# Optimization experiments

Measured on AMD Instinct MI355X. Metric: run time of the kernel, lower is better.

The kernel has to match this reference:

```python
import jax, jax.numpy as jnp
import numpy as np

N = 100000

def _gcn_norm(edge_index, n):
    row, col = edge_index[0], edge_index[1]
    deg = jnp.zeros((n,), jnp.float32).at[col].add(1.0)
    dinv = jnp.where(deg > 0, jax.lax.rsqrt(jnp.maximum(deg, 1.0)), 0.0)
    return dinv[row] * dinv[col]


def _arma_conv(x, row, col, norm, init_w, w, root_w, bias):
    # x: [N, Fin]; init_w: [K, Fin, F]; w: [T-1, K, F, F]; root_w: [T, K, Fin, F]; bias: [T, K, 1, F]
    out = jnp.einsum('nf,kfg->kng', x, init_w)  # [K, N, F]
    T = root_w.shape[0]
    for t in range(T):
        if t > 0:
            out = jnp.einsum('kng,kgh->knh', out, w[t - 1])
        msg = out[:, row, :] * norm[None, :, None]          # [K, E, F] gather
        out = jnp.zeros_like(out).at[:, col, :].add(msg)    # scatter-add to targets
        out = out + jnp.einsum('nf,kfg->kng', x, root_w[t]) + bias[t]
        out = jax.nn.relu(out)
    return out.mean(axis=0)  # average over stacks K


def setup_inputs() -> dict:
    key = jax.random.key(0)
    ks = jax.random.split(key, 12)
    E, Fin, H, C, K = 1600000, 128, 64, 41, 2
    s = 0.1
    return {
        'x': jax.random.normal(ks[0], (N, Fin), jnp.float32),
        'edge_index': jax.random.randint(ks[1], (2, E), 0, N, jnp.int64),
        'w1_init': jax.random.normal(ks[2], (K, Fin, H), jnp.float32) * s,
        'w1': jax.random.normal(ks[3], (1, K, H, H), jnp.float32) * s,
        'w1_root': jax.random.normal(ks[4], (2, K, Fin, H), jnp.float32) * s,
        'b1': jax.random.normal(ks[5], (2, K, 1, H), jnp.float32) * s,
        'w2_init': jax.random.normal(ks[6], (K, H, C), jnp.float32) * s,
        'w2': jax.random.normal(ks[7], (1, K, C, C), jnp.float32) * s,
        'w2_root': jax.random.normal(ks[8], (2, K, H, C), jnp.float32) * s,
        'b2': jax.random.normal(ks[9], (2, K, 1, C), jnp.float32) * s,
    }


def reference(x, edge_index, w1_init, w1, w1_root, b1, w2_init, w2, w2_root, b2):
    row, col = edge_index[0], edge_index[1]
    norm = _gcn_norm(edge_index, N)
    h = jax.nn.relu(_arma_conv(x, row, col, norm, w1_init, w1, w1_root, b1))
    # F.dropout is identity in eval mode
    h = _arma_conv(h, row, col, norm, w2_init, w2, w2_root, b2)
    return jax.nn.log_softmax(h, axis=1)
```

## Files before the change

kernel.cpp:

```cpp
#include <hip/hip_runtime.h>
#include <math.h>

#define TPB 256
typedef unsigned short ushort_t;
typedef unsigned int uint_t;
typedef __attribute__((ext_vector_type(8))) short bf16x8;
typedef __attribute__((ext_vector_type(4))) float f32x4;

__device__ __forceinline__ float bf2f(ushort_t h) {
    return __uint_as_float(((uint_t)h) << 16);
}
__device__ __forceinline__ ushort_t f2bf(float f) {
    uint_t u = __float_as_uint(f);
    u += 0x7fff + ((u >> 16) & 1);
    return (ushort_t)(u >> 16);
}
__device__ __forceinline__ uint_t pack2(float x, float y) {
    return (uint_t)f2bf(x) | ((uint_t)f2bf(y) << 16);
}

#define SWZ_A 32768
#define SWZ_B 24576
#define SWZ_C 12288
#define SWZ_D 12288

__global__ __launch_bounds__(256)
void pre1(const int* __restrict__ col, int* __restrict__ cnt, unsigned short* __restrict__ pos,
          int E, int nEb,
          const float* __restrict__ w1_init, const float* __restrict__ w1,
          const float* __restrict__ w1_root, const float* __restrict__ w2_init,
          const float* __restrict__ w2, const float* __restrict__ w2_root,
          short* __restrict__ swzdst, int nSb,
          const float4* __restrict__ x, uint2* __restrict__ xh, int n4) {
    int b = blockIdx.x;
    if (b < nEb) {
        int e = b * 256 + threadIdx.x;
        if (e < E) pos[e] = (unsigned short)atomicAdd(&cnt[col[e]], 1);
        return;
    }
    if (b < nEb + nSb) {
        int idx = (b - nEb) * 256 + threadIdx.x;
        int region, base, CH, CT;
        if (idx < SWZ_A)                          { region = 0; base = 0; CH = 4; CT = 8; }
        else if (idx < SWZ_A + SWZ_B)             { region = 1; base = SWZ_A; CH = 6; CT = 4; }
        else if (idx < SWZ_A + SWZ_B + SWZ_C)     { region = 2; base = SWZ_A + SWZ_B; CH = 2; CT = 6; }
        else if (idx < SWZ_A + SWZ_B + SWZ_C + SWZ_D)
                                                  { region = 3; base = SWZ_A + SWZ_B + SWZ_C; CH = 4; CT = 3; }
        else return;
        int r = idx - base;
        int j = r & 7, ln = (r >> 3) & 63;
        int rest = r >> 9;
        int ct = rest % CT, c = (rest / CT) % CH, k = rest / (CT * CH);
        int colm = ct * 16 + (ln & 15);
        int kl = (ln >> 4) * 8 + j;
        float v = 0.0f;
        if (region == 0) {
            int kk = c * 32 + kl;
            if (colm < 64)       v = w1_init[((size_t)k * 128 + kk) * 64 + colm];
            else                 v = w1_root[((size_t)k * 128 + kk) * 64 + (colm - 64)];
        } else if (region == 1) {
            if (c < 2) { int kk = c * 32 + kl;        v = w1[((size_t)k * 64 + kk) * 64 + colm]; }
            else       { int kk = (c - 2) * 32 + kl;  v = w1_root[((size_t)(2 + k) * 128 + kk) * 64 + colm]; }
        } else if (region == 2) {
            int kk = c * 32 + kl;
            if (colm < 48) { if (colm < 41)           v = w2_init[((size_t)k * 64 + kk) * 41 + colm]; }
            else           { int c2 = colm - 48; if (c2 < 41) v = w2_root[((size_t)k * 64 + kk) * 41 + c2]; }
        } else {
            if (c < 2) { int kk = c * 32 + kl;       if (kk < 41 && colm < 41) v = w2[((size_t)k * 41 + kk) * 41 + colm]; }
            else       { int kk = (c - 2) * 32 + kl; if (colm < 41)            v = w2_root[((size_t)(2 + k) * 64 + kk) * 41 + colm]; }
        }
        swzdst[(size_t)base + r] = (short)f2bf(v);
        return;
    }
    int i = (b - nEb - nSb) * 256 + threadIdx.x;
    if (i < n4) {
        float4 v = x[i];
        xh[i] = make_uint2(pack2(v.x, v.y), pack2(v.z, v.w));
    }
}

__global__ void scan_block(const int* __restrict__ cnt, int* __restrict__ incl,
                           int* __restrict__ bsum, int N) {
    __shared__ int s[TPB];
    int i = blockIdx.x * TPB + threadIdx.x;
    s[threadIdx.x] = (i < N) ? ((cnt[i] + 3) & ~3) : 0;
    __syncthreads();
    for (int d = 1; d < TPB; d <<= 1) {
        int t = (threadIdx.x >= d) ? s[threadIdx.x - d] : 0;
        __syncthreads();
        s[threadIdx.x] += t;
        __syncthreads();
    }
    if (i < N) incl[i] = s[threadIdx.x];
    if (threadIdx.x == TPB - 1) bsum[blockIdx.x] = s[TPB - 1];
}

__global__ void scan_bsums(int* __restrict__ bsum, int nb) {
    __shared__ int s[512];
    int t = threadIdx.x;
    int v = (t < nb) ? bsum[t] : 0;
    s[t] = v;
    __syncthreads();
    for (int d = 1; d < 512; d <<= 1) {
        int u = (t >= d) ? s[t - d] : 0;
        __syncthreads();
        s[t] += u;
        __syncthreads();
    }
    if (t < nb) bsum[t] = s[t] - v;
}

__global__ void finalize_csr(const int* __restrict__ incl, const int* __restrict__ bsum,
                             const int* __restrict__ cnt, int* __restrict__ rowstart,
                             float* __restrict__ dinv, int N) {
    int i = blockIdx.x * TPB + threadIdx.x;
    if (i < N) {
        rowstart[i + 1] = incl[i] + bsum[blockIdx.x];
        int d = cnt[i];
        dinv[i] = (d > 0) ? rsqrtf((float)d) : 0.0f;
    }
    if (i == 0) rowstart[0] = 0;
}

__global__ void fill_csr(const int* __restrict__ row, const int* __restrict__ col,
                         const int* __restrict__ rowstart, const unsigned short* __restrict__ pos,
                         int* __restrict__ srcidx, int E) {
    int e = blockIdx.x * blockDim.x + threadIdx.x;
    if (e < E) srcidx[rowstart[col[e]] + (int)pos[e]] = row[e];
}

__global__ void pad_csr(const int* __restrict__ rowstart, const int* __restrict__ cnt,
                        int* __restrict__ srcidx, int N) {
    int i = blockIdx.x * blockDim.x + threadIdx.x;
    if (i >= N) return;
    int b = rowstart[i] + cnt[i], en = rowstart[i + 1];
    for (int e = b; e < en; ++e) srcidx[e] = N;
}

template<int CT, int CTA, int CH>
__global__ __launch_bounds__(256, 4)
void gemm_t0(const ushort_t* __restrict__ s2, int s2s, const short* __restrict__ fragbuf,
             const float* __restrict__ biasB, const float* __restrict__ dinv,
             int FB, int N, uint_t* __restrict__ pre, uint_t* __restrict__ outH) {
    constexpr int PP = (CT - CTA) * 8;
    constexpr int PA = CTA * 8;
    const int k = blockIdx.y;
    const int n0 = blockIdx.x * 128;
    const int t = threadIdx.x;
    const int w = t >> 6, lane = t & 63, quad = lane >> 4, lr = lane & 15;
    const short* fb = fragbuf + (size_t)k * CH * CT * 512;

    int r0 = n0 + w * 32 + lr;
    int m0 = r0 < N ? r0 : N - 1;
    int m1 = (r0 + 16) < N ? (r0 + 16) : N - 1;

    bf16x8 a0v[CH], a1v[CH];
#pragma unroll
    for (int c = 0; c < CH; ++c) {
        int off = c * 32 + quad * 8;
        a0v[c] = *(const bf16x8*)&s2[(size_t)m0 * s2s + off];
        a1v[c] = *(const bf16x8*)&s2[(size_t)m1 * s2s + off];
    }

    __shared__ short lds_b[CH * CT * 512];
    {
        constexpr int CHUNKS = CH * CT * 64;
#pragma unroll
        for (int i = 0; i < (CHUNKS + 255) / 256; ++i) {
            int idx = i * 256 + t;
            if (CHUNKS % 256 == 0 || idx < CHUNKS)
                *(bf16x8*)&lds_b[idx * 8] = *(const bf16x8*)&fb[(size_t)idx * 8];
        }
    }
    __syncthreads();

    f32x4 acc[2][CT];
#pragma unroll
    for (int rt = 0; rt < 2; ++rt)
#pragma unroll
        for (int ct = 0; ct < CT; ++ct) acc[rt][ct] = (f32x4){0.f, 0.f, 0.f, 0.f};

#pragma unroll
    for (int c = 0; c < CH; ++c) {
#pragma unroll
        for (int ct = 0; ct < CT; ++ct) {
            bf16x8 bfr = *(const bf16x8*)&lds_b[((size_t)c * CT + ct) * 512 + lane * 8];
            acc[0][ct] = __builtin_amdgcn_mfma_f32_16x16x32_bf16(a0v[c], bfr, acc[0][ct], 0, 0, 0);
            acc[1][ct] = __builtin_amdgcn_mfma_f32_16x16x32_bf16(a1v[c], bfr, acc[1][ct], 0, 0, 0);
        }
    }

#pragma unroll
    for (int rt = 0; rt < 2; ++rt) {
#pragma unroll
        for (int i = 0; i < 4; ++i) {
            int n = n0 + w * 32 + rt * 16 + quad * 4 + i;
            if (n >= N) continue;
            float dnv = dinv[n];
#pragma unroll
            for (int ct = 0; ct < CT; ++ct) {
                int col = ct * 16 + lr;
                float v = acc[rt][ct][i];
                if (ct < CTA) {
                    v *= dnv;
                } else {
                    int c2 = col - CTA * 16;
                    if (c2 < FB) v += biasB[(size_t)k * FB + c2];
                }
                float vn = __shfl_xor(v, 1);
                uint_t p = pack2(v, vn);
                uint_t p2 = __shfl_xor(p, 2);
                if (!(lr & 3)) {
                    if (ct < CTA) {
                        *(uint2*)&outH[((size_t)n * 2 + k) * PA + (col >> 1)] = make_uint2(p, p2);
                    } else {
                        int c2 = col - CTA * 16;
                        *(uint2*)&pre[((size_t)n * 2 + k) * PP + (c2 >> 1)] = make_uint2(p, p2);
                    }
                }
            }
        }
    }
}

__global__ __launch_bounds__(256, 3)
void gemm_t1_l1(const ushort_t* __restrict__ s1, const ushort_t* __restrict__ xh,
                const short* __restrict__ fragbuf, const float* __restrict__ bias,
                int N, uint_t* __restrict__ hhU) {
    constexpr int CT = 4, CH = 6;
    const int n0 = blockIdx.x * 128;
    const int t = threadIdx.x;
    const int w = t >> 6, lane = t & 63, quad = lane >> 4, lr = lane & 15;

    int r0 = n0 + w * 32 + lr;
    int m0 = r0 < N ? r0 : N - 1;
    int m1 = (r0 + 16) < N ? (r0 + 16) : N - 1;

    bf16x8 s0a[2][2], s1a[2][2];
    bf16x8 x0a[4], x1a[4];
#pragma unroll
    for (int c = 0; c < 2; ++c) {
        int off = c * 32 + quad * 8;
#pragma unroll
        for (int kk = 0; kk < 2; ++kk) {
            s0a[c][kk] = *(const bf16x8*)&s1[((size_t)m0 * 2 + kk) * 64 + off];
            s1a[c][kk] = *(const bf16x8*)&s1[((size_t)m1 * 2 + kk) * 64 + off];
        }
    }
#pragma unroll
    for (int c = 0; c < 4; ++c) {
        int off = c * 32 + quad * 8;
        x0a[c] = *(const bf16x8*)&xh[(size_t)m0 * 128 + off];
        x1a[c] = *(const bf16x8*)&xh[(size_t)m1 * 128 + off];
    }

    __shared__ short lds_b[2 * CH * CT * 512];
    {
        constexpr int CHUNKS = 2 * CH * CT * 64;
#pragma unroll
        for (int i = 0; i < CHUNKS / 256; ++i) {
            int idx = i * 256 + t;
            *(bf16x8*)&lds_b[idx * 8] = *(const bf16x8*)&fragbuf[(size_t)idx * 8];
        }
    }
    __syncthreads();

    f32x4 acc[2][2][CT];
#pragma unroll
    for (int k = 0; k < 2; ++k)
#pragma unroll
        for (int rt = 0; rt < 2; ++rt)
#pragma unroll
            for (int ct = 0; ct < CT; ++ct) acc[k][rt][ct] = (f32x4){0.f, 0.f, 0.f, 0.f};

#pragma unroll
    for (int c = 0; c < CH; ++c) {
#pragma unroll
        for (int k = 0; k < 2; ++k) {
            bf16x8 a0 = (c < 2) ? s0a[c][k] : x0a[c - 2];
            bf16x8 a1 = (c < 2) ? s1a[c][k] : x1a[c - 2];
#pragma unroll
            for (int ct = 0; ct < CT; ++ct) {
                bf16x8 b = *(const bf16x8*)&lds_b[(((size_t)k * CH + c) * CT + ct) * 512 + lane * 8];
                acc[k][0][ct] = __builtin_amdgcn_mfma_f32_16x16x32_bf16(a0, b, acc[k][0][ct], 0, 0, 0);
                acc[k][1][ct] = __builtin_amdgcn_mfma_f32_16x16x32_bf16(a1, b, acc[k][1][ct], 0, 0, 0);
            }
        }
    }

#pragma unroll
    for (int rt = 0; rt < 2; ++rt) {
#pragma unroll
        for (int i = 0; i < 4; ++i) {
            int n = n0 + w * 32 + rt * 16 + quad * 4 + i;
            if (n >= N) continue;
#pragma unroll
            for (int ct = 0; ct < CT; ++ct) {
                int col = ct * 16 + lr;
                float v0 = fmaxf(acc[0][rt][ct][i] + bias[col], 0.0f);
                float v1 = fmaxf(acc[1][rt][ct][i] + bias[64 + col], 0.0f);
                float m = 0.5f * (v0 + v1);
                float mn = __shfl_xor(m, 1);
                uint_t p = pack2(m, mn);
                uint_t p2 = __shfl_xor(p, 2);
                if (!(lr & 3)) *(uint2*)&hhU[(size_t)n * 32 + (col >> 1)] = make_uint2(p, p2);
            }
        }
    }
}

__global__ __launch_bounds__(256, 3)
void gemm_t1_l2(const ushort_t* __restrict__ s1, const ushort_t* __restrict__ hh,
                const short* __restrict__ fragbuf, const float* __restrict__ bias,
                int N, float* __restrict__ out) {
    constexpr int CT = 3, CH = 4;
    const int n0 = blockIdx.x * 128;
    const int t = threadIdx.x;
    const int w = t >> 6, lane = t & 63, quad = lane >> 4, lr = lane & 15;

    int r0 = n0 + w * 32 + lr;
    int m0 = r0 < N ? r0 : N - 1;
    int m1 = (r0 + 16) < N ? (r0 + 16) : N - 1;

    bf16x8 s0a[2][2], s1a[2][2];
    bf16x8 h0a[2], h1a[2];
#pragma unroll
    for (int c = 0; c < 2; ++c) {
        int off = c * 32 + quad * 8;
#pragma unroll
        for (int kk = 0; kk < 2; ++kk) {
            s0a[c][kk] = *(const bf16x8*)&s1[((size_t)m0 * 2 + kk) * 48 + off];
            s1a[c][kk] = *(const bf16x8*)&s1[((size_t)m1 * 2 + kk) * 48 + off];
        }
    }
#pragma unroll
    for (int c = 0; c < 2; ++c) {
        int off = c * 32 + quad * 8;
        h0a[c] = *(const bf16x8*)&hh[(size_t)m0 * 64 + off];
        h1a[c] = *(const bf16x8*)&hh[(size_t)m1 * 64 + off];
    }

    __shared__ short lds_b[2 * CH * CT * 512];
    {
        constexpr int CHUNKS = 2 * CH * CT * 64;
#pragma unroll
        for (int i = 0; i < CHUNKS / 256; ++i) {
            int idx = i * 256 + t;
            *(bf16x8*)&lds_b[idx * 8] = *(const bf16x8*)&fragbuf[(size_t)idx * 8];
        }
    }
    __syncthreads();

    f32x4 acc[2][2][CT];
#pragma unroll
    for (int k = 0; k < 2; ++k)
#pragma unroll
        for (int rt = 0; rt < 2; ++rt)
#pragma unroll
            for (int ct = 0; ct < CT; ++ct) acc[k][rt][ct] = (f32x4){0.f, 0.f, 0.f, 0.f};

#pragma unroll
    for (int c = 0; c < CH; ++c) {
#pragma unroll
        for (int k = 0; k < 2; ++k) {
            bf16x8 a0 = (c < 2) ? s0a[c][k] : h0a[c - 2];
            bf16x8 a1 = (c < 2) ? s1a[c][k] : h1a[c - 2];
#pragma unroll
            for (int ct = 0; ct < CT; ++ct) {
                bf16x8 b = *(const bf16x8*)&lds_b[(((size_t)k * CH + c) * CT + ct) * 512 + lane * 8];
                acc[k][0][ct] = __builtin_amdgcn_mfma_f32_16x16x32_bf16(a0, b, acc[k][0][ct], 0, 0, 0);
                acc[k][1][ct] = __builtin_amdgcn_mfma_f32_16x16x32_bf16(a1, b, acc[k][1][ct], 0, 0, 0);
            }
        }
    }

#pragma unroll
    for (int rt = 0; rt < 2; ++rt) {
#pragma unroll
        for (int i = 0; i < 4; ++i) {
            int n = n0 + w * 32 + rt * 16 + quad * 4 + i;
            float m[CT];
            float mx = -1e30f;
#pragma unroll
            for (int ct = 0; ct < CT; ++ct) {
                int col = ct * 16 + lr;
                float b0 = (col < 41) ? bias[col] : 0.0f;
                float b1v = (col < 41) ? bias[41 + col] : 0.0f;
                float v0 = fmaxf(acc[0][rt][ct][i] + b0, 0.0f);
                float v1 = fmaxf(acc[1][rt][ct][i] + b1v, 0.0f);
                m[ct] = 0.5f * (v0 + v1);
                if (col < 41) mx = fmaxf(mx, m[ct]);
            }
#pragma unroll
            for (int msk = 1; msk < 16; msk <<= 1) mx = fmaxf(mx, __shfl_xor(mx, msk));
            float s = 0.0f;
#pragma unroll
            for (int ct = 0; ct < CT; ++ct) {
                int col = ct * 16 + lr;
                if (col < 41) s += __expf(m[ct] - mx);
            }
#pragma unroll
            for (int msk = 1; msk < 16; msk <<= 1) s += __shfl_xor(s, msk);
            float ls = __logf(s);
            if (n < N) {
#pragma unroll
                for (int ct = 0; ct < CT; ++ct) {
                    int col = ct * 16 + lr;
                    if (col < 41) out[(size_t)n * 41 + col] = m[ct] - mx - ls;
                }
            }
        }
    }
}

template<bool SCALE_OUT>
__global__ __launch_bounds__(256)
void gather32(const int* __restrict__ rowstart, const int* __restrict__ srcidx,
              const float* __restrict__ dinv, const uint_t* __restrict__ msg,
              const uint_t* __restrict__ pre, uint_t* __restrict__ outH, int N) {
    int gt = blockIdx.x * 256 + threadIdx.x;
    int n = gt >> 6;
    if (n >= N) return;
    const uint_t lo = (uint_t)(gt & 63);
    const int STR = 64;
    int beg = rowstart[n], end = rowstart[n + 1];
    float dn = dinv[n];
    size_t o = (size_t)n * STR + lo;
    uint_t p = 0;
    if (pre) p = pre[o];

    float ax0 = 0.f, ax1 = 0.f, ay0 = 0.f, ay1 = 0.f;
    int e = beg;
    for (; e + 8 <= end; e += 8) {
        int4 sa = *(const int4*)&srcidx[e];
        int4 sb = *(const int4*)&srcidx[e + 4];
        uint_t m0 = msg[(uint_t)(sa.x * STR) + lo];
        uint_t m1 = msg[(uint_t)(sa.y * STR) + lo];
        uint_t m2 = msg[(uint_t)(sa.z * STR) + lo];
        uint_t m3 = msg[(uint_t)(sa.w * STR) + lo];
        uint_t m4 = msg[(uint_t)(sb.x * STR) + lo];
        uint_t m5 = msg[(uint_t)(sb.y * STR) + lo];
        uint_t m6 = msg[(uint_t)(sb.z * STR) + lo];
        uint_t m7 = msg[(uint_t)(sb.w * STR) + lo];
        ax0 += __uint_as_float(m0 << 16); ay0 += __uint_as_float(m0 & 0xffff0000u);
        ax1 += __uint_as_float(m1 << 16); ay1 += __uint_as_float(m1 & 0xffff0000u);
        ax0 += __uint_as_float(m2 << 16); ay0 += __uint_as_float(m2 & 0xffff0000u);
        ax1 += __uint_as_float(m3 << 16); ay1 += __uint_as_float(m3 & 0xffff0000u);
        ax0 += __uint_as_float(m4 << 16); ay0 += __uint_as_float(m4 & 0xffff0000u);
        ax1 += __uint_as_float(m5 << 16); ay1 += __uint_as_float(m5 & 0xffff0000u);
        ax0 += __uint_as_float(m6 << 16); ay0 += __uint_as_float(m6 & 0xffff0000u);
        ax1 += __uint_as_float(m7 << 16); ay1 += __uint_as_float(m7 & 0xffff0000u);
    }
    if (e < end) {
        int4 sa = *(const int4*)&srcidx[e];
        uint_t m0 = msg[(uint_t)(sa.x * STR) + lo];
        uint_t m1 = msg[(uint_t)(sa.y * STR) + lo];
        uint_t m2 = msg[(uint_t)(sa.z * STR) + lo];
        uint_t m3 = msg[(uint_t)(sa.w * STR) + lo];
        ax0 += __uint_as_float(m0 << 16); ay0 += __uint_as_float(m0 & 0xffff0000u);
        ax1 += __uint_as_float(m1 << 16); ay1 += __uint_as_float(m1 & 0xffff0000u);
        ax0 += __uint_as_float(m2 << 16); ay0 += __uint_as_float(m2 & 0xffff0000u);
        ax1 += __uint_as_float(m3 << 16); ay1 += __uint_as_float(m3 & 0xffff0000u);
    }
    float ax = (ax0 + ax1) * dn;
    float ay = (ay0 + ay1) * dn;
    if (pre) {
        ax = fmaxf(ax + bf2f((ushort_t)p), 0.0f);
        ay = fmaxf(ay + bf2f((ushort_t)(p >> 16)), 0.0f);
    }
    if (SCALE_OUT) { ax *= dn; ay *= dn; }
    outH[o] = pack2(ax, ay);
}

template<bool SCALE_OUT>
__global__ __launch_bounds__(256)
void gather24(const int* __restrict__ rowstart, const int* __restrict__ srcidx,
              const float* __restrict__ dinv, const uint_t* __restrict__ msg,
              const uint_t* __restrict__ pre, uint_t* __restrict__ outH, int N) {
    int gt = blockIdx.x * 256 + threadIdx.x;
    int n = gt / 48;
    if (n >= N) return;
    const uint_t lo = (uint_t)(gt - n * 48);
    const int STR = 48;
    int beg = rowstart[n], end = rowstart[n + 1];
    float dn = dinv[n];
    size_t o = (size_t)n * STR + lo;
    uint_t p = 0;
    if (pre) p = pre[o];

    float ax0 = 0.f, ax1 = 0.f, ay0 = 0.f, ay1 = 0.f;
    int e = beg;
    for (; e + 8 <= end; e += 8) {
        int4 sa = *(const int4*)&srcidx[e];
        int4 sb = *(const int4*)&srcidx[e + 4];
        uint_t m0 = msg[(uint_t)(sa.x * STR) + lo];
        uint_t m1 = msg[(uint_t)(sa.y * STR) + lo];
        uint_t m2 = msg[(uint_t)(sa.z * STR) + lo];
        uint_t m3 = msg[(uint_t)(sa.w * STR) + lo];
        uint_t m4 = msg[(uint_t)(sb.x * STR) + lo];
        uint_t m5 = msg[(uint_t)(sb.y * STR) + lo];
        uint_t m6 = msg[(uint_t)(sb.z * STR) + lo];
        uint_t m7 = msg[(uint_t)(sb.w * STR) + lo];
        ax0 += __uint_as_float(m0 << 16); ay0 += __uint_as_float(m0 & 0xffff0000u);
        ax1 += __uint_as_float(m1 << 16); ay1 += __uint_as_float(m1 & 0xffff0000u);
        ax0 += __uint_as_float(m2 << 16); ay0 += __uint_as_float(m2 & 0xffff0000u);
        ax1 += __uint_as_float(m3 << 16); ay1 += __uint_as_float(m3 & 0xffff0000u);
        ax0 += __uint_as_float(m4 << 16); ay0 += __uint_as_float(m4 & 0xffff0000u);
        ax1 += __uint_as_float(m5 << 16); ay1 += __uint_as_float(m5 & 0xffff0000u);
        ax0 += __uint_as_float(m6 << 16); ay0 += __uint_as_float(m6 & 0xffff0000u);
        ax1 += __uint_as_float(m7 << 16); ay1 += __uint_as_float(m7 & 0xffff0000u);
    }
    if (e < end) {
        int4 sa = *(const int4*)&srcidx[e];
        uint_t m0 = msg[(uint_t)(sa.x * STR) + lo];
        uint_t m1 = msg[(uint_t)(sa.y * STR) + lo];
        uint_t m2 = msg[(uint_t)(sa.z * STR) + lo];
        uint_t m3 = msg[(uint_t)(sa.w * STR) + lo];
        ax0 += __uint_as_float(m0 << 16); ay0 += __uint_as_float(m0 & 0xffff0000u);
        ax1 += __uint_as_float(m1 << 16); ay1 += __uint_as_float(m1 & 0xffff0000u);
        ax0 += __uint_as_float(m2 << 16); ay0 += __uint_as_float(m2 & 0xffff0000u);
        ax1 += __uint_as_float(m3 << 16); ay1 += __uint_as_float(m3 & 0xffff0000u);
    }
    float ax = (ax0 + ax1) * dn;
    float ay = (ay0 + ay1) * dn;
    if (pre) {
        ax = fmaxf(ax + bf2f((ushort_t)p), 0.0f);
        ay = fmaxf(ay + bf2f((ushort_t)(p >> 16)), 0.0f);
    }
    if (SCALE_OUT) { ax *= dn; ay *= dn; }
    outH[o] = pack2(ax, ay);
}

extern "C" void kernel_launch(void* const* d_in, const int* in_sizes, int n_in,
                              void* d_out, int out_size, void* d_ws, size_t ws_size,
                              hipStream_t stream) {
    const float* x       = (const float*)d_in[0];
    const int*   ei      = (const int*)  d_in[1];
    const float* w1_init = (const float*)d_in[2];
    const float* w1      = (const float*)d_in[3];
    const float* w1_root = (const float*)d_in[4];
    const float* b1      = (const float*)d_in[5];
    const float* w2_init = (const float*)d_in[6];
    const float* w2      = (const float*)d_in[7];
    const float* w2_root = (const float*)d_in[8];
    const float* b2      = (const float*)d_in[9];

    const int Fin1 = 128;
    int N = in_sizes[0] / Fin1;
    int E = in_sizes[1] / 2;
    const int* row = ei;
    const int* col = ei + E;

    char* ws = (char*)d_ws;
    size_t off = 0;
    auto carve = [&](size_t bytes) -> void* {
        void* p = ws + off;
        off += (bytes + 255) & ~(size_t)255;
        return p;
    };
    int nblkN = (N + TPB - 1) / TPB;
    int*      cnt      = (int*)     carve((size_t)N * 4);
    int*      incl     = (int*)     carve((size_t)N * 4);
    int*      rowstart = (int*)     carve((size_t)(N + 1) * 4);
    int*      bsum     = (int*)     carve((size_t)nblkN * 4);
    float*    dinv     = (float*)   carve((size_t)N * 4);
    unsigned short* pos = (unsigned short*)carve((size_t)E * 2);
    int*      srcidx   = (int*)     carve((size_t)(E + 3 * (size_t)N + 64) * 4);
    short*    swz      = (short*)   carve((size_t)(SWZ_A + SWZ_B + SWZ_C + SWZ_D) * 2);
    ushort_t* xh       = (ushort_t*)carve((size_t)N * 128 * 2);
    ushort_t* hh       = (ushort_t*)carve((size_t)N * 64 * 2);
    ushort_t* b16A     = (ushort_t*)carve((size_t)N * 2 * 64 * 2 + 256);
    ushort_t* b16B     = (ushort_t*)carve((size_t)N * 2 * 64 * 2 + 256);
    uint_t*   pre      = (uint_t*)  carve((size_t)N * 2 * 32 * 4);

    hipMemsetAsync((char*)b16A + (size_t)N * 256, 0, 256, stream);
    hipMemsetAsync((char*)b16B + (size_t)N * 256, 0, 256, stream);
    hipMemsetAsync(cnt, 0, (size_t)N * 4, stream);

    int nEb = (E + TPB - 1) / TPB;
    int swztot = SWZ_A + SWZ_B + SWZ_C + SWZ_D;
    int nSb = (swztot + TPB - 1) / TPB;
    int n4 = N * 128 / 4;
    int nCb = (n4 + TPB - 1) / TPB;
    pre1<<<nEb + nSb + nCb, TPB, 0, stream>>>(col, cnt, pos, E, nEb,
                                              w1_init, w1, w1_root, w2_init, w2, w2_root,
                                              swz, nSb, (const float4*)x, (uint2*)xh, n4);

    scan_block  <<<nblkN, TPB, 0, stream>>>(cnt, incl, bsum, N);
    scan_bsums  <<<1, 512, 0, stream>>>(bsum, nblkN);
    finalize_csr<<<nblkN, TPB, 0, stream>>>(incl, bsum, cnt, rowstart, dinv, N);
    pad_csr     <<<nblkN, TPB, 0, stream>>>(rowstart, cnt, srcidx, N);
    fill_csr    <<<(E + TPB - 1) / TPB, TPB, 0, stream>>>(row, col, rowstart, pos, srcidx, E);

    const short* swzA = swz;
    const short* swzB = swz + SWZ_A;
    const short* swzC = swz + SWZ_A + SWZ_B;
    const short* swzD = swz + SWZ_A + SWZ_B + SWZ_C;
    dim3 gg2((N + 127) / 128, 2);
    dim3 gg1((N + 127) / 128, 1);
    int g32 = (N * 64 + TPB - 1) / TPB;
    int g24 = (N * 48 + TPB - 1) / TPB;

    gemm_t0<8, 4, 4><<<gg2, TPB, 0, stream>>>(xh, 128, swzA, b1, dinv, 64, N, pre, (uint_t*)b16A);
    gather32<true ><<<g32, TPB, 0, stream>>>(rowstart, srcidx, dinv, (const uint_t*)b16A,
                                             pre, (uint_t*)b16B, N);
    gather32<false><<<g32, TPB, 0, stream>>>(rowstart, srcidx, dinv, (const uint_t*)b16B,
                                             nullptr, (uint_t*)b16A, N);
    gemm_t1_l1<<<gg1, TPB, 0, stream>>>(b16A, xh, swzB, b1 + 2 * 64, N, (uint_t*)hh);

    hipMemsetAsync((char*)b16A + (size_t)N * 192, 0, 192, stream);
    hipMemsetAsync((char*)b16B + (size_t)N * 192, 0, 192, stream);

    gemm_t0<6, 3, 2><<<gg2, TPB, 0, stream>>>(hh, 64, swzC, b2, dinv, 41, N, pre, (uint_t*)b16A);
    gather24<true ><<<g24, TPB, 0, stream>>>(rowstart, srcidx, dinv, (const uint_t*)b16A,
                                             pre, (uint_t*)b16B, N);
    gather24<false><<<g24, TPB, 0, stream>>>(rowstart, srcidx, dinv, (const uint_t*)b16B,
                                             nullptr, (uint_t*)b16A, N);
    gemm_t1_l2<<<gg1, TPB, 0, stream>>>(b16A, hh, swzD, b2 + 2 * 41, N, (float*)d_out);
}
```

Baseline: 571.9 us.

## Fuse layer-1 final GEMM with layer-2 initial GEMM via LDS-staged activations

Merges the last layer-1 GEMM (producing hidden activations) with the first layer-2 GEMM in one kernel, keeping the block's hidden rows in shared memory instead of re-reading them from global memory. Buffer roles for the subsequent gathers are swapped accordingly. The gather kernel also broadcasts per-node CSR bounds and dinv via readfirstlane. This removes a launch and a global read at the cost of a longer kernel with higher register pressure and a relaxed occupancy hint.

```diff
diff --git a/kernel.cpp b/kernel.cpp
--- a/kernel.cpp
+++ b/kernel.cpp
@@ -223,14 +223,19 @@
     }
 }
 
-__global__ __launch_bounds__(256, 3)
-void gemm_t1_l1(const ushort_t* __restrict__ s1, const ushort_t* __restrict__ xh,
-                const short* __restrict__ fragbuf, const float* __restrict__ bias,
-                int N, uint_t* __restrict__ hhU) {
-    constexpr int CT = 4, CH = 6;
+__global__ __launch_bounds__(256)
+void gemm_mid(const ushort_t* __restrict__ s1, const ushort_t* __restrict__ xh,
+              const short* __restrict__ fragB1, const short* __restrict__ fragB2,
+              const float* __restrict__ bias1, const float* __restrict__ bias2,
+              const float* __restrict__ dinv, int N,
+              uint_t* __restrict__ hhU, uint_t* __restrict__ pre, uint_t* __restrict__ outH2) {
+    constexpr int CT1 = 4, CH1 = 6;
+    constexpr int CT2 = 6, CTA2 = 3, CH2 = 2;
     const int n0 = blockIdx.x * 128;
     const int t = threadIdx.x;
     const int w = t >> 6, lane = t & 63, quad = lane >> 4, lr = lane & 15;
+
+    __shared__ short lds[2 * CH1 * CT1 * 512];
 
     int r0 = n0 + w * 32 + lr;
     int m0 = r0 < N ? r0 : N - 1;
@@ -254,39 +259,42 @@
         x1a[c] = *(const bf16x8*)&xh[(size_t)m1 * 128 + off];
     }
 
-    __shared__ short lds_b[2 * CH * CT * 512];
     {
-        constexpr int CHUNKS = 2 * CH * CT * 64;
+        constexpr int CHUNKS = 2 * CH1 * CT1 * 64;
 #pragma unroll
         for (int i = 0; i < CHUNKS / 256; ++i) {
             int idx = i * 256 + t;
-            *(bf16x8*)&lds_b[idx * 8] = *(const bf16x8*)&fragbuf[(size_t)idx * 8];
+            *(bf16x8*)&lds[idx * 8] = *(const bf16x8*)&fragB1[(size_t)idx * 8];
         }
     }
     __syncthreads();
 
-    f32x4 acc[2][2][CT];
+    f32x4 acc[2][2][CT1];
 #pragma unroll
     for (int k = 0; k < 2; ++k)
 #pragma unroll
         for (int rt = 0; rt < 2; ++rt)
 #pragma unroll
-            for (int ct = 0; ct < CT; ++ct) acc[k][rt][ct] = (f32x4){0.f, 0.f, 0.f, 0.f};
-
-#pragma unroll
-    for (int c = 0; c < CH; ++c) {
+            for (int ct = 0; ct < CT1; ++ct) acc[k][rt][ct] = (f32x4){0.f, 0.f, 0.f, 0.f};
+
+#pragma unroll
+    for (int c = 0; c < CH1; ++c) {
 #pragma unroll
         for (int k = 0; k < 2; ++k) {
             bf16x8 a0 = (c < 2) ? s0a[c][k] : x0a[c - 2];
             bf16x8 a1 = (c < 2) ? s1a[c][k] : x1a[c - 2];
 #pragma unroll
-            for (int ct = 0; ct < CT; ++ct) {
-                bf16x8 b = *(const bf16x8*)&lds_b[(((size_t)k * CH + c) * CT + ct) * 512 + lane * 8];
+            for (int ct = 0; ct < CT1; ++ct) {
+                bf16x8 b = *(const bf16x8*)&lds[(((size_t)k * CH1 + c) * CT1 + ct) * 512 + lane * 8];
                 acc[k][0][ct] = __builtin_amdgcn_mfma_f32_16x16x32_bf16(a0, b, acc[k][0][ct], 0, 0, 0);
                 acc[k][1][ct] = __builtin_amdgcn_mfma_f32_16x16x32_bf16(a1, b, acc[k][1][ct], 0, 0, 0);
             }
         }
     }
+    __syncthreads();
+
+    short* lds_h = lds;
+    short* ldsB2 = lds + 8192;
 
 #pragma unroll
     for (int rt = 0; rt < 2; ++rt) {
@@ -295,15 +303,93 @@
             int n = n0 + w * 32 + rt * 16 + quad * 4 + i;
             if (n >= N) continue;
 #pragma unroll
-            for (int ct = 0; ct < CT; ++ct) {
+            for (int ct = 0; ct < CT1; ++ct) {
                 int col = ct * 16 + lr;
-                float v0 = fmaxf(acc[0][rt][ct][i] + bias[col], 0.0f);
-                float v1 = fmaxf(acc[1][rt][ct][i] + bias[64 + col], 0.0f);
+                float v0 = fmaxf(acc[0][rt][ct][i] + bias1[col], 0.0f);
+                float v1 = fmaxf(acc[1][rt][ct][i] + bias1[64 + col], 0.0f);
                 float m = 0.5f * (v0 + v1);
                 float mn = __shfl_xor(m, 1);
                 uint_t p = pack2(m, mn);
                 uint_t p2 = __shfl_xor(p, 2);
-                if (!(lr & 3)) *(uint2*)&hhU[(size_t)n * 32 + (col >> 1)] = make_uint2(p, p2);
+                if (!(lr & 3)) {
+                    *(uint2*)&hhU[(size_t)n * 32 + (col >> 1)] = make_uint2(p, p2);
+                    *(uint2*)&lds_h[(size_t)(n - n0) * 64 + col] = make_uint2(p, p2);
+                }
+            }
+        }
+    }
+
+    {
+        constexpr int CHUNKS2 = 2 * CH2 * CT2 * 64;
+#pragma unroll
+        for (int i = 0; i < CHUNKS2 / 256; ++i) {
+            int idx = i * 256 + t;
+            *(bf16x8*)&ldsB2[idx * 8] = *(const bf16x8*)&fragB2[(size_t)idx * 8];
+        }
+    }
+    __syncthreads();
+
+    int l0 = m0 - n0, l1 = m1 - n0;
+    bf16x8 a20[CH2], a21[CH2];
+#pragma unroll
+    for (int c = 0; c < CH2; ++c) {
+        int off = c * 32 + quad * 8;
+        a20[c] = *(const bf16x8*)&lds_h[(size_t)l0 * 64 + off];
+        a21[c] = *(const bf16x8*)&lds_h[(size_t)l1 * 64 + off];
+    }
+
+    f32x4 acc2[2][2][CT2];
+#pragma unroll
+    for (int k = 0; k < 2; ++k)
+#pragma unroll
+        for (int rt = 0; rt < 2; ++rt)
+#pragma unroll
+            for (int ct = 0; ct < CT2; ++ct) acc2[k][rt][ct] = (f32x4){0.f, 0.f, 0.f, 0.f};
+
+#pragma unroll
+    for (int c = 0; c < CH2; ++c) {
+#pragma unroll
+        for (int k = 0; k < 2; ++k) {
+#pragma unroll
+            for (int ct = 0; ct < CT2; ++ct) {
+                bf16x8 b = *(const bf16x8*)&ldsB2[(((size_t)k * CH2 + c) * CT2 + ct) * 512 + lane * 8];
+                acc2[k][0][ct] = __builtin_amdgcn_mfma_f32_16x16x32_bf16(a20[c], b, acc2[k][0][ct], 0, 0, 0);
+                acc2[k][1][ct] = __builtin_amdgcn_mfma_f32_16x16x32_bf16(a21[c], b, acc2[k][1][ct], 0, 0, 0);
+            }
+        }
+    }
+
+#pragma unroll
+    for (int k = 0; k < 2; ++k) {
+#pragma unroll
+        for (int rt = 0; rt < 2; ++rt) {
+#pragma unroll
+            for (int i = 0; i < 4; ++i) {
+                int n = n0 + w * 32 + rt * 16 + quad * 4 + i;
+                if (n >= N) continue;
+                float dnv = dinv[n];
+#pragma unroll
+                for (int ct = 0; ct < CT2; ++ct) {
+                    int col = ct * 16 + lr;
+                    float v = acc2[k][rt][ct][i];
+                    if (ct < CTA2) {
+                        v *= dnv;
+                    } else {
+                        int c2 = col - CTA2 * 16;
+                        if (c2 < 41) v += bias2[(size_t)k * 41 + c2];
+                    }
+                    float vn = __shfl_xor(v, 1);
+                    uint_t p = pack2(v, vn);
+                    uint_t p2 = __shfl_xor(p, 2);
+                    if (!(lr & 3)) {
+                        if (ct < CTA2) {
+                            *(uint2*)&outH2[((size_t)n * 2 + k) * 24 + (col >> 1)] = make_uint2(p, p2);
+                        } else {
+                            int c2 = col - CTA2 * 16;
+                            *(uint2*)&pre[((size_t)n * 2 + k) * 24 + (c2 >> 1)] = make_uint2(p, p2);
+                        }
+                    }
+                }
             }
         }
     }
@@ -423,8 +509,9 @@
     if (n >= N) return;
     const uint_t lo = (uint_t)(gt & 63);
     const int STR = 64;
-    int beg = rowstart[n], end = rowstart[n + 1];
-    float dn = dinv[n];
+    int beg = __builtin_amdgcn_readfirstlane(rowstart[n]);
+    int end = __builtin_amdgcn_readfirstlane(rowstart[n + 1]);
+    float dn = __uint_as_float(__builtin_amdgcn_readfirstlane(__float_as_uint(dinv[n])));
     size_t o = (size_t)n * STR + lo;
     uint_t p = 0;
     if (pre) p = pre[o];
@@ -606,15 +693,16 @@
                                              pre, (uint_t*)b16B, N);
     gather32<false><<<g32, TPB, 0, stream>>>(rowstart, srcidx, dinv, (const uint_t*)b16B,
                                              nullptr, (uint_t*)b16A, N);
-    gemm_t1_l1<<<gg1, TPB, 0, stream>>>(b16A, xh, swzB, b1 + 2 * 64, N, (uint_t*)hh);
+
+    gemm_mid<<<gg1, TPB, 0, stream>>>(b16A, xh, swzB, swzC, b1 + 2 * 64, b2, dinv, N,
+                                      (uint_t*)hh, pre, (uint_t*)b16B);
 
     hipMemsetAsync((char*)b16A + (size_t)N * 192, 0, 192, stream);
     hipMemsetAsync((char*)b16B + (size_t)N * 192, 0, 192, stream);
 
-    gemm_t0<6, 3, 2><<<gg2, TPB, 0, stream>>>(hh, 64, swzC, b2, dinv, 41, N, pre, (uint_t*)b16A);
-    gather24<true ><<<g24, TPB, 0, stream>>>(rowstart, srcidx, dinv, (const uint_t*)b16A,
-                                             pre, (uint_t*)b16B, N);
-    gather24<false><<<g24, TPB, 0, stream>>>(rowstart, srcidx, dinv, (const uint_t*)b16B,
-                                             nullptr, (uint_t*)b16A, N);
-    gemm_t1_l2<<<gg1, TPB, 0, stream>>>(b16A, hh, swzD, b2 + 2 * 41, N, (float*)d_out);
-}
+    gather24<true ><<<g24, TPB, 0, stream>>>(rowstart, srcidx, dinv, (const uint_t*)b16B,
+                                             pre, (uint_t*)b16A, N);
+    gather24<false><<<g24, TPB, 0, stream>>>(rowstart, srcidx, dinv, (const uint_t*)b16A,
+                                             nullptr, (uint_t*)b16B, N);
+    gemm_t1_l2<<<gg1, TPB, 0, stream>>>(b16B, hh, swzD, b2 + 2 * 41, N, (float*)d_out);
+}
```

Measured after the change: 560.9 us. About the same (-1.9%).
